# Optimization experiments

Hardware: AMD Instinct MI355X
Metric: run time of the kernel (lower is better)

Reference implementation:

```python
import jax, jax.numpy as jnp
import numpy as np

L1 = 513          # max_data_length + 1
EMB = 64          # embedding_dim (w)
V = 6             # num_tokens
B = 128           # batch

def setup_inputs() -> dict:
    key = jax.random.key(0)
    k1, k2, k3 = jax.random.split(key, 3)
    src = jax.random.randint(k1, (B, L1), 0, V, dtype=jnp.int64)
    # nn.Embedding default init: N(0,1)
    embedding = jax.random.normal(k2, (V, EMB), dtype=jnp.float32)
    # xavier_uniform over (L1, EMB, L1, V): fan_in = EMB*L1*V? torch treats dim0 as fan_out... use gain scale ~ sqrt(6/(fan_in+fan_out)) with fan computed on flattened dims
    fan_in = EMB * L1 * V
    fan_out = L1
    bound = float(np.sqrt(6.0 / (fan_in + fan_out)))
    weight = jax.random.uniform(k3, (L1, EMB, L1, V), dtype=jnp.float32, minval=-bound, maxval=bound)
    bias = jnp.zeros((L1, V), dtype=jnp.float32)
    return {"src": src, "embedding": embedding, "weight": weight, "bias": bias}

def reference(src, embedding, weight, bias):
    # embedding lookup: (B, L1, EMB)
    x = embedding[src].astype(jnp.float32)
    # causal mask over (s, t): lower-triangular ones
    mask = jnp.tril(jnp.ones((L1, L1), dtype=jnp.float32))
    # batched masked trilinear contraction -> (B, L1, V)
    out = jnp.einsum('bsw,swtv,st->btv', x, weight, mask)
    out = out + bias[None, :, :]
    # permute to (B, V, L1)
    return jnp.transpose(out, (0, 2, 1))
```

## Files before the change

### kernel.cpp

```cpp
#include <hip/hip_runtime.h>
#include <hip/hip_bf16.h>

#define L1C 513
#define EMBC 64
#define VC 6
#define BC 128
#define NCOLS (L1C * VC)
#define NTC 64
#define NTILES ((NCOLS + NTC - 1) / NTC)
#define CSC 13
#define NCHUNK ((L1C + CSC - 1) / CSC)

#define XELEMS ((size_t)L1C * BC * EMBC)
#define XBYTES (XELEMS * 2)
#define OUTELEMS ((size_t)BC * NCOLS)
#define PARTBYTES (OUTELEMS * 2)

typedef __attribute__((ext_vector_type(8))) short short8;
typedef __attribute__((ext_vector_type(4))) float f32x4;

__device__ __forceinline__ unsigned int pack_bf16x2(float a, float b) {
    __hip_bfloat16 ha = __float2bfloat16(a);
    __hip_bfloat16 hb = __float2bfloat16(b);
    unsigned short ua, ub;
    __builtin_memcpy(&ua, &ha, 2);
    __builtin_memcpy(&ub, &hb, 2);
    return (unsigned int)ua | ((unsigned int)ub << 16);
}

__device__ __forceinline__ unsigned short bf16bits(float a) {
    __hip_bfloat16 h = __float2bfloat16(a);
    unsigned short u;
    __builtin_memcpy(&u, &h, 2);
    return u;
}

__global__ void init_out_kernel(float* __restrict__ out, const float* __restrict__ bias) {
    int i = blockIdx.x * 256 + threadIdx.x;
    if (i >= (int)OUTELEMS) return;
    int r = i % NCOLS;
    int v = r / L1C;
    int t = r - v * L1C;
    out[i] = bias[t * VC + v];
}

__global__ void build_x_kernel(const int* __restrict__ src, const float* __restrict__ emb,
                               unsigned short* __restrict__ X) {
    const int s = blockIdx.x;
    const int b = threadIdx.x >> 1;
    const int half = threadIdx.x & 1;
    const int tok = src[b * L1C + s];
    const float2* e = (const float2*)(emb + tok * EMBC + half * 32);
    unsigned int* row = (unsigned int*)(X + ((size_t)s * BC + b) * EMBC) + half * 16;
#pragma unroll
    for (int i = 0; i < 16; ++i) {
        float2 f = e[i];
        row[i] = pack_bf16x2(f.x, f.y);
    }
}

template <bool PARTIAL>
__global__ __launch_bounds__(256, 4) void gemm_tril_kernel(
    const float* __restrict__ Wt, const unsigned short* __restrict__ X,
    void* __restrict__ outp, int CS) {
    const int xb = blockIdx.x;
    const int xcd = xb & 7;
    const int pos = xb >> 3;
    const int tile = ((xcd == 0) ? 0 : (7 + (xcd - 1) * 6)) + pos;

    const int chunk = blockIdx.y;
    const int n0 = tile * NTC;
    const int s0 = chunk * CS;
    const int sEnd = min(s0 + CS, L1C);
    const int sBeg = max(s0, n0 / VC);
    if (sBeg >= sEnd) return;

    __shared__ __align__(16) unsigned short Blds[2][NTC * EMBC];

    const int tid = threadIdx.x;
    const int wid = tid >> 6;
    const int lane = tid & 63;
    const int l15 = lane & 15;
    const int h = lane >> 4;

    const int n = n0 + lane;
    const int tcol = n / VC;
    const size_t nsafe = (n < NCOLS) ? (size_t)n : (size_t)(NCOLS - 1);
    const int wrow0 = wid * 16;

    f32x4 acc[2][4];
#pragma unroll
    for (int i = 0; i < 2; ++i)
#pragma unroll
        for (int j = 0; j < 4; ++j) acc[i][j] = f32x4{0.f, 0.f, 0.f, 0.f};

#define SYNCB()                                                \
    {                                                          \
        __builtin_amdgcn_sched_barrier(0);                     \
        asm volatile("s_waitcnt lgkmcnt(0)" ::: "memory");     \
        __builtin_amdgcn_s_barrier();                          \
        __builtin_amdgcn_sched_barrier(0);                     \
    }

#define ISSUEW(ss, farr)                                                         \
    {                                                                            \
        const float* wb_ = Wt + ((size_t)(ss) * EMBC + wrow0) * NCOLS + nsafe;   \
        _Pragma("unroll") for (int u_ = 0; u_ < 16; ++u_)                        \
            farr[u_] = wb_[(size_t)u_ * NCOLS];                                  \
    }

#define PACKW(ss, farr, buf)                                                     \
    {                                                                            \
        const bool act_ = (tcol <= (ss));                                        \
        char* dr_ = (char*)Blds[buf] + lane * 128;                               \
        const int sw_ = (lane & 15) << 3;                                        \
        _Pragma("unroll") for (int u_ = 0; u_ < 4; ++u_) {                       \
            float g0 = act_ ? farr[u_ * 4 + 0] : 0.f;                            \
            float g1 = act_ ? farr[u_ * 4 + 1] : 0.f;                            \
            float g2 = act_ ? farr[u_ * 4 + 2] : 0.f;                            \
            float g3 = act_ ? farr[u_ * 4 + 3] : 0.f;                            \
            uint2 pk_ = make_uint2(pack_bf16x2(g0, g1), pack_bf16x2(g2, g3));    \
            *(uint2*)(dr_ + ((wid * 32 + u_ * 8) ^ sw_)) = pk_;                  \
        }                                                                        \
    }

#define ISSUEA(ss, aarr)                                                             \
    {                                                                                \
        const int scl_ = ((ss) < L1C) ? (ss) : (L1C - 1);                            \
        const unsigned short* xr_ = X + (size_t)scl_ * (BC * EMBC);                  \
        aarr[0] = *(const short8*)(xr_ + (wid * 32 + l15) * EMBC + h * 8);           \
        aarr[1] = *(const short8*)(xr_ + (wid * 32 + l15) * EMBC + 32 + h * 8);      \
        aarr[2] = *(const short8*)(xr_ + (wid * 32 + 16 + l15) * EMBC + h * 8);      \
        aarr[3] = *(const short8*)(xr_ + (wid * 32 + 16 + l15) * EMBC + 32 + h * 8); \
    }

#define MFMASTEP(aarr, buf)                                                                          \
    {                                                                                                \
        const int sw_ = l15 << 3;                                                                    \
        _Pragma("unroll") for (int kk_ = 0; kk_ < 2; ++kk_) {                                        \
            _Pragma("unroll") for (int nt_ = 0; nt_ < 4; ++nt_) {                                    \
                const char* rb_ = (const char*)Blds[buf] + (nt_ * 16 + l15) * 128;                   \
                const int c0_ = (kk_ * 64 + h * 16) ^ sw_;                                           \
                short8 bb_;                                                                          \
                __builtin_memcpy(&bb_, rb_ + c0_, 8);                                                \
                __builtin_memcpy((char*)&bb_ + 8, rb_ + (c0_ ^ 8), 8);                               \
                acc[0][nt_] = __builtin_amdgcn_mfma_f32_16x16x32_bf16(aarr[kk_], bb_, acc[0][nt_], 0, 0, 0);     \
                acc[1][nt_] = __builtin_amdgcn_mfma_f32_16x16x32_bf16(aarr[2 + kk_], bb_, acc[1][nt_], 0, 0, 0); \
            }                                                                                        \
        }                                                                                            \
    }

    {
        float fW0[16], fW1[16];
        short8 aC[4];
        ISSUEW(sBeg, fW1);
        PACKW(sBeg, fW1, 0);
        ISSUEA(sBeg, aC);
        if (sBeg + 1 < sEnd) ISSUEW(sBeg + 1, fW0);
        SYNCB();

        int s = sBeg, cur = 0;
        while (true) {
            if (s + 2 < sEnd) ISSUEW(s + 2, fW1);
            MFMASTEP(aC, cur);
            if (s + 1 < sEnd) {
                ISSUEA(s + 1, aC);
                PACKW(s + 1, fW0, cur ^ 1);
            }
            SYNCB();
            cur ^= 1;
            if (++s >= sEnd) break;

            if (s + 2 < sEnd) ISSUEW(s + 2, fW0);
            MFMASTEP(aC, cur);
            if (s + 1 < sEnd) {
                ISSUEA(s + 1, aC);
                PACKW(s + 1, fW1, cur ^ 1);
            }
            SYNCB();
            cur ^= 1;
            if (++s >= sEnd) break;
        }
    }

#pragma unroll
    for (int nt = 0; nt < 4; ++nt) {
        const int nn = n0 + nt * 16 + l15;
        if (nn >= NCOLS) continue;
        if (PARTIAL) {
            unsigned short* dst = (unsigned short*)outp + (size_t)chunk * OUTELEMS;
#pragma unroll
            for (int ms = 0; ms < 2; ++ms)
#pragma unroll
                for (int r = 0; r < 4; ++r) {
                    const int bi = wid * 32 + ms * 16 + h * 4 + r;
                    dst[(size_t)bi * NCOLS + nn] = bf16bits(acc[ms][nt][r]);
                }
        } else {
            float* dst = (float*)outp;
            const int t = nn / VC;
            const int v = nn - t * VC;
            const size_t obase = (size_t)v * L1C + t;
#pragma unroll
            for (int ms = 0; ms < 2; ++ms)
#pragma unroll
                for (int r = 0; r < 4; ++r) {
                    const int bi = wid * 32 + ms * 16 + h * 4 + r;
                    atomicAdd(dst + (size_t)bi * NCOLS + obase, acc[ms][nt][r]);
                }
        }
    }
#undef SYNCB
#undef ISSUEW
#undef PACKW
#undef ISSUEA
#undef MFMASTEP
}

__global__ void reduce_kernel(const unsigned short* __restrict__ partial,
                              const float* __restrict__ bias,
                              float* __restrict__ out, int nchunks, int CS) {
    int i4 = blockIdx.x * 256 + threadIdx.x;
    if (i4 >= (int)(OUTELEMS / 4)) return;
    const size_t base = (size_t)i4 * 4;
    float sum[4];
    int cf[4];
    int cmin = 1 << 30;
#pragma unroll
    for (int j = 0; j < 4; ++j) {
        int idx = (int)base + j;
        int nn = idx % NCOLS;
        sum[j] = bias[nn];
        int tl = nn >> 6;
        int tmin = (tl << 6) / VC;
        cf[j] = tmin / CS;
        cmin = min(cmin, cf[j]);
    }
    for (int c = cmin; c < nchunks; ++c) {
        const ushort4 p = *(const ushort4*)(partial + (size_t)c * OUTELEMS + base);
        unsigned int u0 = (unsigned int)p.x << 16, u1 = (unsigned int)p.y << 16;
        unsigned int u2 = (unsigned int)p.z << 16, u3 = (unsigned int)p.w << 16;
        float f0, f1, f2, f3;
        __builtin_memcpy(&f0, &u0, 4);
        __builtin_memcpy(&f1, &u1, 4);
        __builtin_memcpy(&f2, &u2, 4);
        __builtin_memcpy(&f3, &u3, 4);
        if (c >= cf[0]) sum[0] += f0;
        if (c >= cf[1]) sum[1] += f1;
        if (c >= cf[2]) sum[2] += f2;
        if (c >= cf[3]) sum[3] += f3;
    }
#pragma unroll
    for (int j = 0; j < 4; ++j) {
        int idx = (int)base + j;
        int b = idx / NCOLS;
        int nn = idx - b * NCOLS;
        int t = nn / VC;
        int v = nn - t * VC;
        out[(size_t)b * NCOLS + (size_t)v * L1C + t] = sum[j];
    }
}

extern "C" void kernel_launch(void* const* d_in, const int* in_sizes, int n_in,
                              void* d_out, int out_size, void* d_ws, size_t ws_size,
                              hipStream_t stream) {
    const int* src = (const int*)d_in[0];
    const float* emb = (const float*)d_in[1];
    const float* wt = (const float*)d_in[2];
    const float* bias = (const float*)d_in[3];
    float* out = (float*)d_out;
    unsigned short* X = (unsigned short*)d_ws;

    build_x_kernel<<<L1C, 256, 0, stream>>>(src, emb, X);

    if (ws_size >= XBYTES + (size_t)NCHUNK * PARTBYTES) {
        unsigned short* partial = (unsigned short*)((char*)d_ws + XBYTES);
        dim3 grid(NTILES, NCHUNK);
        gemm_tril_kernel<true><<<grid, 256, 0, stream>>>(wt, X, (void*)partial, CSC);
        reduce_kernel<<<(int)((OUTELEMS / 4 + 255) / 256), 256, 0, stream>>>(partial, bias, out, NCHUNK, CSC);
    } else if (ws_size >= XBYTES + 2 * PARTBYTES) {
        int nchunks = (int)((ws_size - XBYTES) / PARTBYTES);
        if (nchunks > NCHUNK) nchunks = NCHUNK;
        int CS = (L1C + nchunks - 1) / nchunks;
        nchunks = (L1C + CS - 1) / CS;
        unsigned short* partial = (unsigned short*)((char*)d_ws + XBYTES);
        dim3 grid(NTILES, nchunks);
        gemm_tril_kernel<true><<<grid, 256, 0, stream>>>(wt, X, (void*)partial, CS);
        reduce_kernel<<<(int)((OUTELEMS / 4 + 255) / 256), 256, 0, stream>>>(partial, bias, out, nchunks, CS);
    } else {
        init_out_kernel<<<(int)((OUTELEMS + 255) / 256), 256, 0, stream>>>(out, bias);
        dim3 grid(NTILES, 17);
        gemm_tril_kernel<false><<<grid, 256, 0, stream>>>(wt, X, (void*)out, 31);
    }
}
```

Baseline: 81.60 us.

## Widen N tile to 128 columns with vectorized weight loads and new LDS swizzle

Doubles the column tile per block from 64 to 128, so each wave computes 8 N-subtiles and the loaded activation fragments are reused across more MFMAs. Weight loads switch from scalar per-lane column reads to 16-byte vector loads of 4 adjacent columns, with a new XOR swizzle function to keep LDS writes and reads conflict-free. Launch bounds drop to 2 blocks per CU and the tile-to-XCD mapping and reduce-kernel chunk bounds are updated to match. This raises register pressure and reduces the number of blocks, which may hurt latency hiding and the causal-skip granularity.

Measured after the change: 94.74 us. +16.1%, slower.

```diff
diff --git a/kernel.cpp b/kernel.cpp
--- a/kernel.cpp
+++ b/kernel.cpp
@@ -6,7 +6,7 @@
 #define VC 6
 #define BC 128
 #define NCOLS (L1C * VC)
-#define NTC 64
+#define NTC 128
 #define NTILES ((NCOLS + NTC - 1) / NTC)
 #define CSC 13
 #define NCHUNK ((L1C + CSC - 1) / CSC)
@@ -33,6 +33,10 @@
     unsigned short u;
     __builtin_memcpy(&u, &h, 2);
     return u;
+}
+
+__device__ __forceinline__ int swz_slot(int c) {
+    return (c & 12) | ((((c >> 1) ^ (c >> 4)) & 1) << 1) | ((c ^ (c >> 5)) & 1);
 }
 
 __global__ void init_out_kernel(float* __restrict__ out, const float* __restrict__ bias) {
@@ -60,13 +64,13 @@
 }
 
 template <bool PARTIAL>
-__global__ __launch_bounds__(256, 4) void gemm_tril_kernel(
+__global__ __launch_bounds__(256, 2) void gemm_tril_kernel(
     const float* __restrict__ Wt, const unsigned short* __restrict__ X,
     void* __restrict__ outp, int CS) {
     const int xb = blockIdx.x;
     const int xcd = xb & 7;
     const int pos = xb >> 3;
-    const int tile = ((xcd == 0) ? 0 : (7 + (xcd - 1) * 6)) + pos;
+    const int tile = ((xcd == 0) ? 0 : (4 + (xcd - 1) * 3)) + pos;
 
     const int chunk = blockIdx.y;
     const int n0 = tile * NTC;
@@ -83,16 +87,18 @@
     const int l15 = lane & 15;
     const int h = lane >> 4;
 
-    const int n = n0 + lane;
-    const int tcol = n / VC;
-    const size_t nsafe = (n < NCOLS) ? (size_t)n : (size_t)(NCOLS - 1);
-    const int wrow0 = wid * 16;
-
-    f32x4 acc[2][4];
+    const int k31 = lane & 31;
+    const int c0 = 4 * k31;
+    const int wr0 = wid * 16 + (lane >> 5) * 8;
+    int tc[4];
+#pragma unroll
+    for (int j = 0; j < 4; ++j) tc[j] = (n0 + c0 + j) / VC;
+
+    f32x4 acc[2][8];
 #pragma unroll
     for (int i = 0; i < 2; ++i)
 #pragma unroll
-        for (int j = 0; j < 4; ++j) acc[i][j] = f32x4{0.f, 0.f, 0.f, 0.f};
+        for (int j = 0; j < 8; ++j) acc[i][j] = f32x4{0.f, 0.f, 0.f, 0.f};
 
 #define SYNCB()                                                \
     {                                                          \
@@ -102,26 +108,38 @@
         __builtin_amdgcn_sched_barrier(0);                     \
     }
 
-#define ISSUEW(ss, farr)                                                         \
-    {                                                                            \
-        const float* wb_ = Wt + ((size_t)(ss) * EMBC + wrow0) * NCOLS + nsafe;   \
-        _Pragma("unroll") for (int u_ = 0; u_ < 16; ++u_)                        \
-            farr[u_] = wb_[(size_t)u_ * NCOLS];                                  \
-    }
-
-#define PACKW(ss, farr, buf)                                                     \
-    {                                                                            \
-        const bool act_ = (tcol <= (ss));                                        \
-        char* dr_ = (char*)Blds[buf] + lane * 128;                               \
-        const int sw_ = (lane & 15) << 3;                                        \
-        _Pragma("unroll") for (int u_ = 0; u_ < 4; ++u_) {                       \
-            float g0 = act_ ? farr[u_ * 4 + 0] : 0.f;                            \
-            float g1 = act_ ? farr[u_ * 4 + 1] : 0.f;                            \
-            float g2 = act_ ? farr[u_ * 4 + 2] : 0.f;                            \
-            float g3 = act_ ? farr[u_ * 4 + 3] : 0.f;                            \
-            uint2 pk_ = make_uint2(pack_bf16x2(g0, g1), pack_bf16x2(g2, g3));    \
-            *(uint2*)(dr_ + ((wid * 32 + u_ * 8) ^ sw_)) = pk_;                  \
-        }                                                                        \
+#define ISSUEW(ss, farr)                                                            \
+    {                                                                               \
+        const float* wb_ = Wt + (size_t)((ss) * EMBC + wr0) * NCOLS;                \
+        if (n0 + c0 + 4 <= NCOLS) {                                                 \
+            _Pragma("unroll") for (int i_ = 0; i_ < 8; ++i_)                        \
+                __builtin_memcpy(&farr[i_][0], wb_ + (size_t)i_ * NCOLS + n0 + c0, 16); \
+        } else {                                                                    \
+            _Pragma("unroll") for (int i_ = 0; i_ < 8; ++i_) {                      \
+                _Pragma("unroll") for (int j_ = 0; j_ < 4; ++j_) {                  \
+                    const int cj_ = (n0 + c0 + j_ < NCOLS) ? (n0 + c0 + j_) : (NCOLS - 1); \
+                    farr[i_][j_] = wb_[(size_t)i_ * NCOLS + cj_];                   \
+                }                                                                   \
+            }                                                                       \
+        }                                                                           \
+    }
+
+#define PACKW(ss, farr, buf)                                                        \
+    {                                                                               \
+        _Pragma("unroll") for (int j_ = 0; j_ < 4; ++j_) {                          \
+            const int c_ = c0 + j_;                                                 \
+            const bool act_ = (tc[j_] <= (ss));                                     \
+            const int fsw_ = swz_slot(c_) << 3;                                     \
+            char* dr_ = (char*)Blds[buf] + c_ * 128;                                \
+            _Pragma("unroll") for (int u_ = 0; u_ < 2; ++u_) {                      \
+                float g0 = act_ ? farr[4 * u_ + 0][j_] : 0.f;                       \
+                float g1 = act_ ? farr[4 * u_ + 1][j_] : 0.f;                       \
+                float g2 = act_ ? farr[4 * u_ + 2][j_] : 0.f;                       \
+                float g3 = act_ ? farr[4 * u_ + 3][j_] : 0.f;                       \
+                uint2 pk_ = make_uint2(pack_bf16x2(g0, g1), pack_bf16x2(g2, g3));   \
+                *(uint2*)(dr_ + ((2 * wr0 + 8 * u_) ^ fsw_)) = pk_;                 \
+            }                                                                       \
+        }                                                                           \
     }
 
 #define ISSUEA(ss, aarr)                                                             \
@@ -136,14 +154,15 @@
 
 #define MFMASTEP(aarr, buf)                                                                          \
     {                                                                                                \
-        const int sw_ = l15 << 3;                                                                    \
         _Pragma("unroll") for (int kk_ = 0; kk_ < 2; ++kk_) {                                        \
-            _Pragma("unroll") for (int nt_ = 0; nt_ < 4; ++nt_) {                                    \
-                const char* rb_ = (const char*)Blds[buf] + (nt_ * 16 + l15) * 128;                   \
-                const int c0_ = (kk_ * 64 + h * 16) ^ sw_;                                           \
+            _Pragma("unroll") for (int nt_ = 0; nt_ < 8; ++nt_) {                                    \
+                const int c_ = nt_ * 16 + l15;                                                       \
+                const int fsw_ = swz_slot(c_) << 3;                                                  \
+                const char* rb_ = (const char*)Blds[buf] + c_ * 128;                                 \
+                const int o1_ = (kk_ * 64 + h * 16) ^ fsw_;                                          \
                 short8 bb_;                                                                          \
-                __builtin_memcpy(&bb_, rb_ + c0_, 8);                                                \
-                __builtin_memcpy((char*)&bb_ + 8, rb_ + (c0_ ^ 8), 8);                               \
+                __builtin_memcpy(&bb_, rb_ + o1_, 8);                                                \
+                __builtin_memcpy((char*)&bb_ + 8, rb_ + (o1_ ^ 8), 8);                               \
                 acc[0][nt_] = __builtin_amdgcn_mfma_f32_16x16x32_bf16(aarr[kk_], bb_, acc[0][nt_], 0, 0, 0);     \
                 acc[1][nt_] = __builtin_amdgcn_mfma_f32_16x16x32_bf16(aarr[2 + kk_], bb_, acc[1][nt_], 0, 0, 0); \
             }                                                                                        \
@@ -151,7 +170,7 @@
     }
 
     {
-        float fW0[16], fW1[16];
+        float fW0[8][4], fW1[8][4];
         short8 aC[4];
         ISSUEW(sBeg, fW1);
         PACKW(sBeg, fW1, 0);
@@ -184,7 +203,7 @@
     }
 
 #pragma unroll
-    for (int nt = 0; nt < 4; ++nt) {
+    for (int nt = 0; nt < 8; ++nt) {
         const int nn = n0 + nt * 16 + l15;
         if (nn >= NCOLS) continue;
         if (PARTIAL) {
@@ -231,8 +250,8 @@
         int idx = (int)base + j;
         int nn = idx % NCOLS;
         sum[j] = bias[nn];
-        int tl = nn >> 6;
-        int tmin = (tl << 6) / VC;
+        int tl = nn >> 7;
+        int tmin = (tl << 7) / VC;
         cf[j] = tmin / CS;
         cmin = min(cmin, cf[j]);
     }
```
